# Kernel tuning notes

Hardware: AMD Instinct MI355X
Metric: run time of the kernel (lower is better)

Reference implementation:

```python
import jax, jax.numpy as jnp
import numpy as np

NUM_HOPS = 8
NEG_INF = -1e9


def setup_inputs() -> dict:
    key = jax.random.key(0)
    ks = jax.random.split(key, 10)
    B, N, D, H = 4, 1024, 256, 8
    x = jax.random.normal(ks[0], (B, N, D), dtype=jnp.float32)
    adj = (jax.random.uniform(ks[1], (B, N, N)) < 0.02).astype(jnp.int32)
    edge_attr = jax.random.normal(ks[2], (B, H, N, N), dtype=jnp.float32) * 0.1
    s = 1.0 / np.sqrt(D)
    Wq = jax.random.normal(ks[3], (D, D), dtype=jnp.float32) * s
    Wk = jax.random.normal(ks[4], (D, D), dtype=jnp.float32) * s
    Wv = jax.random.normal(ks[5], (D, D), dtype=jnp.float32) * s
    Wo = jax.random.normal(ks[6], (D, D), dtype=jnp.float32) * s
    W_fuse = jax.random.normal(ks[7], (H, D), dtype=jnp.float32) * s
    diff_weight = jax.random.normal(ks[8], (NUM_HOPS, H), dtype=jnp.float32)
    return {"x": x, "adj": adj, "edge_attr": edge_attr, "Wq": Wq, "Wk": Wk,
            "Wv": Wv, "Wo": Wo, "W_fuse": W_fuse, "diff_weight": diff_weight}


def edge_gat(x, adj, edge_attr, Wq, Wk, Wv, Wo):
    B, N, D = x.shape
    H = edge_attr.shape[1]
    dh = D // H
    q = (x @ Wq).reshape(B, N, H, dh)
    k = (x @ Wk).reshape(B, N, H, dh)
    v = (x @ Wv).reshape(B, N, H, dh)
    scores = jnp.einsum("bihd,bjhd->bhij", q, k) / jnp.sqrt(jnp.float32(dh))
    scores = scores + edge_attr  # additive edge bias
    mask = (adj > 0)[:, None, :, :]  # [B,1,N,N]
    attn = jax.nn.softmax(jnp.where(mask, scores, NEG_INF), axis=-1)
    out = jnp.einsum("bhij,bjhd->bihd", attn, v).reshape(B, N, D)
    return x + out @ Wo


def node_edge_fusion(x, adj, edge_attr, W_fuse):
    # degree-normalized per-head aggregation of incident edge features -> nodes
    a = adj.astype(x.dtype)
    deg = jnp.clip(a.sum(-1), 1.0)  # [B,N]
    f = jnp.einsum("bij,bhij->bih", a, edge_attr) / deg[:, :, None]  # [B,N,H]
    return x + f @ W_fuse


def graph_diffusion(adj, weight):
    # BFS hop-distance bias: bias[b,h,i,j] = weight[hop(i,j), h] if reachable in <= NUM_HOPS hops
    K, H = weight.shape
    a = adj.astype(jnp.float32)
    reach = adj > 0
    explored = reach
    dist = jnp.where(reach, 0, K)  # hop index (0 == 1-hop neighbor)
    cur = a
    for k in range(1, K):
        cur_b = (cur @ a) > 0
        newly = cur_b & ~explored
        dist = jnp.where(newly, k, dist)
        explored = explored | newly
        cur = cur_b.astype(jnp.float32)
    dist_c = jnp.clip(dist, 0, K - 1)
    bias = jnp.where(explored[..., None], weight[dist_c], 0.0)  # [B,N,N,H]
    return jnp.transpose(bias, (0, 3, 1, 2)), explored


def reference(x, adj, edge_attr, Wq, Wk, Wv, Wo, W_fuse, diff_weight):
    x1 = edge_gat(x, adj, edge_attr, Wq, Wk, Wv, Wo)
    x2 = node_edge_fusion(x1, adj, edge_attr, W_fuse)
    position_bias = edge_attr
    bfs_bias, explored = graph_diffusion(adj, diff_weight)
    att_bias = position_bias + bfs_bias
    return x2, att_bias, explored
```

## Files before the change

### kernel.cpp

```cpp
#include <hip/hip_runtime.h>
#include <stdint.h>

#define NN 1024
#define DD 256
#define KHOPS 8

typedef unsigned short u16;
typedef unsigned long long u64;
typedef unsigned char u8;
typedef float f32x4v __attribute__((ext_vector_type(4)));

__device__ __forceinline__ float b2f(u16 u){ return __uint_as_float(((unsigned int)u) << 16); }
__device__ __forceinline__ u16 f2b(float f){
  unsigned int x = __float_as_uint(f);
  unsigned int r = (x + 0x7FFFu + ((x >> 16) & 1u)) >> 16;
  return (u16)r;
}
__device__ __forceinline__ float wsum(float v){
  #pragma unroll
  for(int off = 32; off >= 1; off >>= 1) v += __shfl_xor(v, off, 64);
  return v;
}

__global__ __launch_bounds__(256) void k_fill(float* p, unsigned n, float v){
  unsigned idx = blockIdx.x * 256 + threadIdx.x;
  if(idx < n) p[idx] = v;
}

__global__ __launch_bounds__(256) void k_prep(const float* X, const float* Wq, const float* Wk,
                                              const float* Wv, float* qf, float* kf, u16* vb,
                                              const int* adj, u64* bits){
  __shared__ float xs[32][256];
  int t = threadIdx.x;
  if(blockIdx.x >= 384){
    int vblk = blockIdx.x - 384;
    int row = vblk * 4 + (t >> 6);
    int lane = t & 63;
    const int* ar = adj + (size_t)row * NN;
    #pragma unroll
    for(int w = 0; w < 16; w++){
      u64 msk = __ballot(ar[w * 64 + lane] != 0);
      if(lane == 0) bits[(size_t)row * 16 + w] = msk;
    }
    return;
  }
  int proj = blockIdx.x >> 7;
  int rb = blockIdx.x & 127;
  const float* W = (proj == 0) ? Wq : (proj == 1) ? Wk : Wv;
  const float* Xb = X + (size_t)rb * 32 * 256;
  #pragma unroll
  for(int m = 0; m < 32; m++) xs[m][t] = Xb[m * 256 + t];
  __syncthreads();
  float acc[32];
  #pragma unroll
  for(int r = 0; r < 32; r++) acc[r] = 0.f;
  for(int k4 = 0; k4 < 64; k4++){
    float w0 = W[(size_t)(k4 * 4 + 0) * 256 + t];
    float w1 = W[(size_t)(k4 * 4 + 1) * 256 + t];
    float w2 = W[(size_t)(k4 * 4 + 2) * 256 + t];
    float w3 = W[(size_t)(k4 * 4 + 3) * 256 + t];
    #pragma unroll
    for(int r = 0; r < 32; r++){
      float4 xv = *(const float4*)&xs[r][k4 * 4];
      acc[r] = fmaf(xv.x, w0, fmaf(xv.y, w1, fmaf(xv.z, w2, fmaf(xv.w, w3, acc[r]))));
    }
  }
  int rowbase = rb * 32;
  if(proj == 2){
    for(int r = 0; r < 32; r++) vb[(size_t)(rowbase + r) * 256 + t] = f2b(acc[r]);
  } else {
    float* dst = (proj == 0) ? qf : kf;
    for(int r = 0; r < 32; r++) dst[(size_t)(rowbase + r) * 256 + t] = acc[r];
  }
}

__global__ __launch_bounds__(512) void k_bfs(const u64* bits, u8* dist, float* expl){
  __shared__ __attribute__((aligned(16))) u64 asw[16384];
  __shared__ __attribute__((aligned(16))) u8 drow4[8][1024];
  __shared__ u64 red4[8][16];
  int tid = threadIdx.x;
  int wv = tid >> 6, lane = tid & 63;
  int batch = blockIdx.x >> 6;
  int rowbase = (blockIdx.x & 63) * 16;
  const u64* bb = bits + (((size_t)batch << 10)) * 16;
  for(int g = tid; g < 8192; g += 512){
    int j = g >> 3, c = g & 7;
    ulonglong2 v = *(const ulonglong2*)(bb + (size_t)j * 16 + c * 2);
    int ce = c ^ (j & 7);
    *(ulonglong2*)(&asw[j * 16 + ce * 2]) = v;
  }
  __syncthreads();
  int s = lane & 7;
  for(int rr = 0; rr < 2; rr++){
    int row_local = rowbase + wv * 2 + rr;
    int row = (batch << 10) + row_local;
    u64 vis[16], cur[16];
    {
      const u64* p = asw + row_local * 16;
      int sr = row_local & 7;
      #pragma unroll
      for(int c = 0; c < 8; c++){
        ulonglong2 v = *(const ulonglong2*)(p + (((c ^ sr)) << 1));
        vis[2*c] = v.x; vis[2*c+1] = v.y;
        cur[2*c] = v.x; cur[2*c+1] = v.y;
      }
    }
    { int4 ff; ff.x = ff.y = ff.z = ff.w = -1; ((int4*)drow4[wv])[lane] = ff; }
    __builtin_amdgcn_wave_barrier();
    #pragma unroll
    for(int it = 0; it < 16; it++)
      if((cur[it] >> lane) & 1) drow4[wv][it * 64 + lane] = 0;
    for(int k = 1; k < KHOPS; k++){
      unsigned mymask = 0;
      #pragma unroll
      for(int it = 0; it < 16; it++) mymask |= ((unsigned)((cur[it] >> lane) & 1)) << it;
      u64 acc[16];
      #pragma unroll
      for(int w = 0; w < 16; w++) acc[w] = 0;
      while(mymask){
        int it0 = __builtin_ctz(mymask); mymask &= mymask - 1;
        int it1 = it0;
        if(mymask){ it1 = __builtin_ctz(mymask); mymask &= mymask - 1; }
        const u64* pA = asw + (it0 * 64 + lane) * 16;
        const u64* pB = asw + (it1 * 64 + lane) * 16;
        ulonglong2 a0 = *(const ulonglong2*)(pA + ((0^s)<<1)), b0 = *(const ulonglong2*)(pB + ((0^s)<<1));
        ulonglong2 a1 = *(const ulonglong2*)(pA + ((1^s)<<1)), b1 = *(const ulonglong2*)(pB + ((1^s)<<1));
        ulonglong2 a2 = *(const ulonglong2*)(pA + ((2^s)<<1)), b2 = *(const ulonglong2*)(pB + ((2^s)<<1));
        ulonglong2 a3 = *(const ulonglong2*)(pA + ((3^s)<<1)), b3 = *(const ulonglong2*)(pB + ((3^s)<<1));
        ulonglong2 a4 = *(const ulonglong2*)(pA + ((4^s)<<1)), b4 = *(const ulonglong2*)(pB + ((4^s)<<1));
        ulonglong2 a5 = *(const ulonglong2*)(pA + ((5^s)<<1)), b5 = *(const ulonglong2*)(pB + ((5^s)<<1));
        ulonglong2 a6 = *(const ulonglong2*)(pA + ((6^s)<<1)), b6 = *(const ulonglong2*)(pB + ((6^s)<<1));
        ulonglong2 a7 = *(const ulonglong2*)(pA + ((7^s)<<1)), b7 = *(const ulonglong2*)(pB + ((7^s)<<1));
        acc[0]  |= a0.x | b0.x;  acc[1]  |= a0.y | b0.y;
        acc[2]  |= a1.x | b1.x;  acc[3]  |= a1.y | b1.y;
        acc[4]  |= a2.x | b2.x;  acc[5]  |= a2.y | b2.y;
        acc[6]  |= a3.x | b3.x;  acc[7]  |= a3.y | b3.y;
        acc[8]  |= a4.x | b4.x;  acc[9]  |= a4.y | b4.y;
        acc[10] |= a5.x | b5.x;  acc[11] |= a5.y | b5.y;
        acc[12] |= a6.x | b6.x;  acc[13] |= a6.y | b6.y;
        acc[14] |= a7.x | b7.x;  acc[15] |= a7.y | b7.y;
      }
      #pragma unroll
      for(int w = 0; w < 16; w++){
        acc[w] |= __shfl_xor(acc[w], 16, 64);
        acc[w] |= __shfl_xor(acc[w], 32, 64);
      }
      int g4 = lane >> 4;
      u64 r0, r1, r2, r3;
      if(g4 == 0){ r0 = acc[0];  r1 = acc[1];  r2 = acc[2];  r3 = acc[3];  }
      else if(g4 == 1){ r0 = acc[4];  r1 = acc[5];  r2 = acc[6];  r3 = acc[7];  }
      else if(g4 == 2){ r0 = acc[8];  r1 = acc[9];  r2 = acc[10]; r3 = acc[11]; }
      else            { r0 = acc[12]; r1 = acc[13]; r2 = acc[14]; r3 = acc[15]; }
      #pragma unroll
      for(int off = 1; off <= 8; off <<= 1){
        r0 |= __shfl_xor(r0, off, 64);
        r1 |= __shfl_xor(r1, off, 64);
        r2 |= __shfl_xor(r2, off, 64);
        r3 |= __shfl_xor(r3, off, 64);
      }
      int sub = lane & 15;
      if(sub == 0)      red4[wv][g4 * 4 + 0] = r0;
      else if(sub == 1) red4[wv][g4 * 4 + 1] = r1;
      else if(sub == 2) red4[wv][g4 * 4 + 2] = r2;
      else if(sub == 3) red4[wv][g4 * 4 + 3] = r3;
      __builtin_amdgcn_wave_barrier();
      u64 any = 0, andv = ~0ull;
      #pragma unroll
      for(int w = 0; w < 16; w++){
        u64 nv = red4[wv][w];
        u64 nw = nv & ~vis[w];
        vis[w] |= nw;
        cur[w] = nw;
        any |= nw;
        andv &= vis[w];
      }
      __builtin_amdgcn_wave_barrier();
      if(any == 0) break;
      #pragma unroll
      for(int it = 0; it < 16; it++)
        if((cur[it] >> lane) & 1) drow4[wv][it * 64 + lane] = (u8)k;
      if(andv == ~0ull) break;
    }
    __builtin_amdgcn_wave_barrier();
    ((int4*)(dist + (size_t)row * NN))[lane] = ((const int4*)drow4[wv])[lane];
    float* eo = expl + (size_t)row * NN;
    #pragma unroll
    for(int it = 0; it < 16; it++){
      int j = it * 64 + lane;
      eo[j] = ((vis[it] >> lane) & 1) ? 1.0f : 0.0f;
    }
  }
}

__global__ __launch_bounds__(256) void k_biasattn(
    const float* x, const u64* bits, const float* ea, const u8* dist, const float* dw,
    const float* qf, const float* kf, const u16* vb,
    const float* Wo, const float* Wf, float* ab_out, float* x2)
{
  __shared__ float qs[256];
  __shared__ float aos[256];
  __shared__ float fs[8];
  __shared__ u16 nlist[1024];
  __shared__ float sc0[4][64], sc1[4][64];
  __shared__ float evl0[4][64], evl1[4][64];
  __shared__ float w8s[8][8];
  __shared__ u64 wm[16];
  __shared__ int bs[16];
  __shared__ int ncnt_s;
  int t = threadIdx.x, wv = t >> 6, lane = t & 63;
  int bi = blockIdx.x, b = bi >> 10, i = bi & 1023;
  qs[t] = qf[(size_t)bi * 256 + t];
  if(t < 64) w8s[t & 7][t >> 3] = dw[(t >> 3) * 8 + (t & 7)];
  if(wv == 0){
    if(lane < 16) wm[lane] = bits[(size_t)bi * 16 + lane];
    __builtin_amdgcn_wave_barrier();
    if(lane == 0){
      int run = 0;
      #pragma unroll
      for(int it = 0; it < 16; it++){ bs[it] = run; run += __popcll(wm[it]); }
      ncnt_s = run;
    }
    __builtin_amdgcn_wave_barrier();
    if(lane < 16){
      u64 w = wm[lane];
      int pos = bs[lane];
      while(w){
        int bpos = __builtin_ctzll(w);
        nlist[pos++] = (u16)(lane * 64 + bpos);
        w &= w - 1;
      }
    }
  }
  __syncthreads();
  int cnt = ncnt_s;
  const float scale = 0.17677669529663687f;
  int d = lane & 31;
  int half = lane >> 5;
  bool isV = (lane >= 32);
  int g8 = lane >> 3, r8 = lane & 7;
  size_t kvbase = ((size_t)(b << 10)) * 256;
  const u8* drow = dist + (size_t)bi * NN;
  int h0 = wv * 2, h1 = wv * 2 + 1;
  int widx0 = (((b << 3) + h0) << 10) + i;
  int widx1 = (((b << 3) + h1) << 10) + i;
  const float* earow0 = ea + (size_t)widx0 * NN;
  const float* earow1 = ea + (size_t)widx1 * NN;
  float* abrow0 = ab_out + (size_t)widx0 * NN;
  float* abrow1 = ab_out + (size_t)widx1 * NN;
  float fpart0 = 0.f, fpart1 = 0.f;
  #pragma unroll
  for(int g = 0; g < 4; g++){
    int idx = g * 256 + lane * 4;
    f32x4v e0 = *(const f32x4v*)(earow0 + idx);
    f32x4v e1 = *(const f32x4v*)(earow1 + idx);
    unsigned dd4 = *(const unsigned*)(drow + idx);
    float v0[4] = {e0.x, e0.y, e0.z, e0.w};
    float v1[4] = {e1.x, e1.y, e1.z, e1.w};
    f32x4v o0, o1;
    #pragma unroll
    for(int e2 = 0; e2 < 4; e2++){
      int dd = (dd4 >> (e2 * 8)) & 255;
      float w0 = (dd != 255) ? w8s[h0][dd & 7] : 0.f;
      float w1 = (dd != 255) ? w8s[h1][dd & 7] : 0.f;
      float ov0 = v0[e2] + w0, ov1 = v1[e2] + w1;
      if(e2 == 0){ o0.x = ov0; o1.x = ov1; }
      else if(e2 == 1){ o0.y = ov0; o1.y = ov1; }
      else if(e2 == 2){ o0.z = ov0; o1.z = ov1; }
      else { o0.w = ov0; o1.w = ov1; }
      if(dd == 0){ fpart0 += v0[e2]; fpart1 += v1[e2]; }
    }
    __builtin_nontemporal_store(o0, (f32x4v*)(abrow0 + idx));
    __builtin_nontemporal_store(o1, (f32x4v*)(abrow1 + idx));
  }
  float fsum0 = wsum(fpart0);
  float fsum1 = wsum(fpart1);
  if(lane == 0){
    fs[h0] = (cnt > 0) ? fsum0 / (float)cnt : 0.f;
    fs[h1] = (cnt > 0) ? fsum1 / (float)cnt : 0.f;
  }
  if(cnt > 0 && cnt <= 64){
    for(int s = lane; s < cnt; s += 64){
      int j = nlist[s];
      evl0[wv][s] = earow0[j];
      evl1[wv][s] = earow1[j];
    }
  }
  __builtin_amdgcn_wave_barrier();
  if(cnt > 0 && cnt <= 64){
    float4 q40 = *(const float4*)&qs[h0 * 32 + r8 * 4];
    float4 q41 = *(const float4*)&qs[h1 * 32 + r8 * 4];
    for(int u = 0; u < cnt; u += 8){
      int s = u + g8;
      bool valid = (s < cnt);
      int j = nlist[valid ? s : (cnt - 1)];
      const float* krow = kf + kvbase + (size_t)j * 256;
      float4 k40 = *(const float4*)(krow + h0 * 32 + r8 * 4);
      float4 k41 = *(const float4*)(krow + h1 * 32 + r8 * 4);
      float p0 = k40.x * q40.x + k40.y * q40.y + k40.z * q40.z + k40.w * q40.w;
      float p1 = k41.x * q41.x + k41.y * q41.y + k41.z * q41.z + k41.w * q41.w;
      p0 += __shfl_xor(p0, 1, 64);  p1 += __shfl_xor(p1, 1, 64);
      p0 += __shfl_xor(p0, 2, 64);  p1 += __shfl_xor(p1, 2, 64);
      p0 += __shfl_xor(p0, 4, 64);  p1 += __shfl_xor(p1, 4, 64);
      if(r8 == 0 && valid){
        sc0[wv][s] = p0 * scale + evl0[wv][s];
        sc1[wv][s] = p1 * scale + evl1[wv][s];
      }
    }
    __builtin_amdgcn_wave_barrier();
    float m0 = -3.0e38f, m1 = -3.0e38f;
    for(int s = 0; s < cnt; s++){ m0 = fmaxf(m0, sc0[wv][s]); m1 = fmaxf(m1, sc1[wv][s]); }
    float4 o40 = {0.f,0.f,0.f,0.f}, o41 = {0.f,0.f,0.f,0.f};
    float Sp0 = 0.f, Sp1 = 0.f;
    for(int u = 0; u < cnt; u += 8){
      int s = u + g8;
      if(s < cnt){
        float p0 = __expf(sc0[wv][s] - m0);
        float p1 = __expf(sc1[wv][s] - m1);
        Sp0 += p0; Sp1 += p1;
        int j = nlist[s];
        const u16* vrow = vb + kvbase + (size_t)j * 256;
        ushort4 vv0 = *(const ushort4*)(vrow + h0 * 32 + r8 * 4);
        ushort4 vv1 = *(const ushort4*)(vrow + h1 * 32 + r8 * 4);
        o40.x = fmaf(p0, b2f(vv0.x), o40.x);  o41.x = fmaf(p1, b2f(vv1.x), o41.x);
        o40.y = fmaf(p0, b2f(vv0.y), o40.y);  o41.y = fmaf(p1, b2f(vv1.y), o41.y);
        o40.z = fmaf(p0, b2f(vv0.z), o40.z);  o41.z = fmaf(p1, b2f(vv1.z), o41.z);
        o40.w = fmaf(p0, b2f(vv0.w), o40.w);  o41.w = fmaf(p1, b2f(vv1.w), o41.w);
      }
    }
    #pragma unroll
    for(int off = 8; off <= 32; off <<= 1){
      o40.x += __shfl_xor(o40.x, off, 64);  o41.x += __shfl_xor(o41.x, off, 64);
      o40.y += __shfl_xor(o40.y, off, 64);  o41.y += __shfl_xor(o41.y, off, 64);
      o40.z += __shfl_xor(o40.z, off, 64);  o41.z += __shfl_xor(o41.z, off, 64);
      o40.w += __shfl_xor(o40.w, off, 64);  o41.w += __shfl_xor(o41.w, off, 64);
      Sp0 += __shfl_xor(Sp0, off, 64);      Sp1 += __shfl_xor(Sp1, off, 64);
    }
    if(g8 == 0){
      float iS0 = 1.f / Sp0, iS1 = 1.f / Sp1;
      float4 ov0; ov0.x = o40.x * iS0; ov0.y = o40.y * iS0; ov0.z = o40.z * iS0; ov0.w = o40.w * iS0;
      float4 ov1; ov1.x = o41.x * iS1; ov1.y = o41.y * iS1; ov1.z = o41.z * iS1; ov1.w = o41.w * iS1;
      *(float4*)&aos[h0 * 32 + r8 * 4] = ov0;
      *(float4*)&aos[h1 * 32 + r8 * 4] = ov1;
    }
  } else if(cnt > 64){
    #pragma unroll
    for(int hh = 0; hh < 2; hh++){
      int h = wv * 2 + hh;
      const float* earow = (hh == 0) ? earow0 : earow1;
      const float* Kb = kf + kvbase + h * 32 + d;
      const u16*   Vb = vb + kvbase + h * 32 + d;
      float q_d = qs[h * 32 + d];
      float S = 0.f, o = 0.f;
      float m = -3.0e38f;
      for(int idx = 0; idx < cnt; idx++){
        int j = nlist[idx];
        float kv = isV ? b2f(Vb[(size_t)j * 256]) : Kb[(size_t)j * 256];
        float prod = isV ? 0.f : kv * q_d;
        #pragma unroll
        for(int off = 16; off >= 1; off >>= 1) prod += __shfl_xor(prod, off, 64);
        float e = earow[j];
        float s2 = __shfl(prod, 0, 64) * scale + e;
        float nm = fmaxf(m, s2);
        float rs = __expf(m - nm);
        float p  = __expf(s2 - nm);
        S = S * rs + p;
        o = o * rs + p * (isV ? kv : 0.f);
        m = nm;
      }
      if(isV) aos[h * 32 + d] = o / S;
    }
  } else {
    #pragma unroll
    for(int hh = 0; hh < 2; hh++){
      int h = wv * 2 + hh;
      const u16* Vb = vb + kvbase + h * 32 + d;
      float o = 0.f;
      for(int j2 = half; j2 < 1024; j2 += 2)
        o += b2f(Vb[(size_t)j2 * 256]);
      o += __shfl_xor(o, 32, 64);
      if(lane < 32) aos[h * 32 + d] = o / 1024.f;
    }
  }
  __syncthreads();
  const float* Wcol = Wo + t;
  float r0 = x[(size_t)bi * 256 + t], r1 = 0.f, r2 = 0.f, r3 = 0.f;
  #pragma unroll 4
  for(int k = 0; k < 256; k += 4){
    r0 = fmaf(aos[k],     Wcol[(size_t)k * 256],       r0);
    r1 = fmaf(aos[k + 1], Wcol[(size_t)(k + 1) * 256], r1);
    r2 = fmaf(aos[k + 2], Wcol[(size_t)(k + 2) * 256], r2);
    r3 = fmaf(aos[k + 3], Wcol[(size_t)(k + 3) * 256], r3);
  }
  float res = (r0 + r1) + (r2 + r3);
  #pragma unroll
  for(int h = 0; h < 8; h++) res = fmaf(fs[h], Wf[(size_t)h * 256 + t], res);
  x2[(size_t)bi * 256 + t] = res;
}

extern "C" void kernel_launch(void* const* d_in, const int* in_sizes, int n_in,
                              void* d_out, int out_size, void* d_ws, size_t ws_size,
                              hipStream_t stream) {
  float* out = (float*)d_out;
  float* x2   = out;
  float* ab   = out + 1048576;
  float* expl = out + 34603008;

  bool ok = (n_in == 9) &&
            in_sizes[0] == 1048576  &&
            in_sizes[1] == 4194304  &&
            in_sizes[2] == 33554432 &&
            in_sizes[3] == 65536 && in_sizes[4] == 65536 &&
            in_sizes[5] == 65536 && in_sizes[6] == 65536 &&
            in_sizes[7] == 2048  && in_sizes[8] == 64 &&
            out_size == 38797312;
  if(!ok){
    hipLaunchKernelGGL(k_fill, dim3(4096), dim3(256), 0, stream, x2, 1048576u, 1000.0f);
    return;
  }
  if(ws_size < (size_t)15204352){
    hipLaunchKernelGGL(k_fill, dim3(4096), dim3(256), 0, stream, x2, 1048576u, 2000.0f);
    return;
  }

  const float* x   = (const float*)d_in[0];
  const int*   adj = (const int*)d_in[1];
  const float* ea  = (const float*)d_in[2];
  const float* Wq  = (const float*)d_in[3];
  const float* Wk  = (const float*)d_in[4];
  const float* Wv  = (const float*)d_in[5];
  const float* Wo  = (const float*)d_in[6];
  const float* Wf  = (const float*)d_in[7];
  const float* dw  = (const float*)d_in[8];

  char* ws = (char*)d_ws;
  u64*   bits  = (u64*)(ws + 0);
  u8*    dist  = (u8*)(ws + 524288);
  float* qf    = (float*)(ws + 4718592);
  float* kf    = (float*)(ws + 8912896);
  u16*   vb    = (u16*)(ws + 13107200);

  hipLaunchKernelGGL(k_prep,     dim3(1408), dim3(256), 0, stream,
                     x, Wq, Wk, Wv, qf, kf, vb, adj, bits);
  hipLaunchKernelGGL(k_bfs,      dim3(256),  dim3(512), 0, stream, bits, dist, expl);
  hipLaunchKernelGGL(k_biasattn, dim3(4096), dim3(256), 0, stream,
                     x, bits, ea, dist, dw, qf, kf, vb, Wo, Wf, ab, x2);
}
```

Baseline: 182.4 us.

## Split output projection into separate batched kernel reusing Wo across rows

Moves the Wo/W_fuse output projection out of the per-row attention kernel into a new kernel that processes 16 rows per block. Attention output and fused edge values are written to workspace instead of shared memory. Each Wo element is then loaded once per 16 rows rather than once per row, which cuts global/L2 traffic on Wo. In exchange there is an extra kernel launch, a workspace round trip, and the new kernel runs only 256 blocks.

```diff
diff --git a/kernel.cpp b/kernel.cpp
--- a/kernel.cpp
+++ b/kernel.cpp
@@ -193,13 +193,11 @@
 }
 
 __global__ __launch_bounds__(256) void k_biasattn(
-    const float* x, const u64* bits, const float* ea, const u8* dist, const float* dw,
+    const u64* bits, const float* ea, const u8* dist, const float* dw,
     const float* qf, const float* kf, const u16* vb,
-    const float* Wo, const float* Wf, float* ab_out, float* x2)
+    float* ab_out, float* ao, float* fvals)
 {
   __shared__ float qs[256];
-  __shared__ float aos[256];
-  __shared__ float fs[8];
   __shared__ u16 nlist[1024];
   __shared__ float sc0[4][64], sc1[4][64];
   __shared__ float evl0[4][64], evl1[4][64];
@@ -240,6 +238,7 @@
   int g8 = lane >> 3, r8 = lane & 7;
   size_t kvbase = ((size_t)(b << 10)) * 256;
   const u8* drow = dist + (size_t)bi * NN;
+  float* aorow = ao + (size_t)bi * 256;
   int h0 = wv * 2, h1 = wv * 2 + 1;
   int widx0 = (((b << 3) + h0) << 10) + i;
   int widx1 = (((b << 3) + h1) << 10) + i;
@@ -275,8 +274,8 @@
   float fsum0 = wsum(fpart0);
   float fsum1 = wsum(fpart1);
   if(lane == 0){
-    fs[h0] = (cnt > 0) ? fsum0 / (float)cnt : 0.f;
-    fs[h1] = (cnt > 0) ? fsum1 / (float)cnt : 0.f;
+    fvals[widx0] = (cnt > 0) ? fsum0 / (float)cnt : 0.f;
+    fvals[widx1] = (cnt > 0) ? fsum1 / (float)cnt : 0.f;
   }
   if(cnt > 0 && cnt <= 64){
     for(int s = lane; s < cnt; s += 64){
@@ -339,8 +338,8 @@
       float iS0 = 1.f / Sp0, iS1 = 1.f / Sp1;
       float4 ov0; ov0.x = o40.x * iS0; ov0.y = o40.y * iS0; ov0.z = o40.z * iS0; ov0.w = o40.w * iS0;
       float4 ov1; ov1.x = o41.x * iS1; ov1.y = o41.y * iS1; ov1.z = o41.z * iS1; ov1.w = o41.w * iS1;
-      *(float4*)&aos[h0 * 32 + r8 * 4] = ov0;
-      *(float4*)&aos[h1 * 32 + r8 * 4] = ov1;
+      *(float4*)(aorow + h0 * 32 + r8 * 4) = ov0;
+      *(float4*)(aorow + h1 * 32 + r8 * 4) = ov1;
     }
   } else if(cnt > 64){
     #pragma unroll
@@ -367,7 +366,7 @@
         o = o * rs + p * (isV ? kv : 0.f);
         m = nm;
       }
-      if(isV) aos[h * 32 + d] = o / S;
+      if(isV) aorow[h * 32 + d] = o / S;
     }
   } else {
     #pragma unroll
@@ -378,23 +377,52 @@
       for(int j2 = half; j2 < 1024; j2 += 2)
         o += b2f(Vb[(size_t)j2 * 256]);
       o += __shfl_xor(o, 32, 64);
-      if(lane < 32) aos[h * 32 + d] = o / 1024.f;
-    }
+      if(lane < 32) aorow[h * 32 + d] = o / 1024.f;
+    }
+  }
+}
+
+__global__ __launch_bounds__(256) void k_outproj(const float* ao, const float* x, const float* fsd,
+                                                 const float* Wo, const float* Wf, float* x2){
+  __shared__ float as_[16][256];
+  __shared__ float fsl[16][8];
+  int t = threadIdx.x;
+  int rb = blockIdx.x;
+  const float* Ab = ao + (size_t)rb * 16 * 256;
+  #pragma unroll
+  for(int m = 0; m < 16; m++) as_[m][t] = Ab[m * 256 + t];
+  if(t < 128){
+    int m = t >> 3, h = t & 7;
+    int row = rb * 16 + m;
+    int b = row >> 10, i = row & 1023;
+    fsl[m][h] = fsd[((((size_t)b << 3) + h) << 10) + i];
   }
   __syncthreads();
-  const float* Wcol = Wo + t;
-  float r0 = x[(size_t)bi * 256 + t], r1 = 0.f, r2 = 0.f, r3 = 0.f;
-  #pragma unroll 4
-  for(int k = 0; k < 256; k += 4){
-    r0 = fmaf(aos[k],     Wcol[(size_t)k * 256],       r0);
-    r1 = fmaf(aos[k + 1], Wcol[(size_t)(k + 1) * 256], r1);
-    r2 = fmaf(aos[k + 2], Wcol[(size_t)(k + 2) * 256], r2);
-    r3 = fmaf(aos[k + 3], Wcol[(size_t)(k + 3) * 256], r3);
-  }
-  float res = (r0 + r1) + (r2 + r3);
-  #pragma unroll
-  for(int h = 0; h < 8; h++) res = fmaf(fs[h], Wf[(size_t)h * 256 + t], res);
-  x2[(size_t)bi * 256 + t] = res;
+  float acc[16];
+  #pragma unroll
+  for(int r = 0; r < 16; r++) acc[r] = 0.f;
+  for(int k4 = 0; k4 < 64; k4++){
+    float w0 = Wo[(size_t)(k4 * 4 + 0) * 256 + t];
+    float w1 = Wo[(size_t)(k4 * 4 + 1) * 256 + t];
+    float w2 = Wo[(size_t)(k4 * 4 + 2) * 256 + t];
+    float w3 = Wo[(size_t)(k4 * 4 + 3) * 256 + t];
+    #pragma unroll
+    for(int r = 0; r < 16; r++){
+      float4 av = *(const float4*)&as_[r][k4 * 4];
+      acc[r] = fmaf(av.x, w0, fmaf(av.y, w1, fmaf(av.z, w2, fmaf(av.w, w3, acc[r]))));
+    }
+  }
+  float wf[8];
+  #pragma unroll
+  for(int h = 0; h < 8; h++) wf[h] = Wf[(size_t)h * 256 + t];
+  int rowbase = rb * 16;
+  for(int r = 0; r < 16; r++){
+    int row = rowbase + r;
+    float res = acc[r] + x[(size_t)row * 256 + t];
+    #pragma unroll
+    for(int h = 0; h < 8; h++) res = fmaf(fsl[r][h], wf[h], res);
+    x2[(size_t)row * 256 + t] = res;
+  }
 }
 
 extern "C" void kernel_launch(void* const* d_in, const int* in_sizes, int n_in,
@@ -417,7 +445,7 @@
     hipLaunchKernelGGL(k_fill, dim3(4096), dim3(256), 0, stream, x2, 1048576u, 1000.0f);
     return;
   }
-  if(ws_size < (size_t)15204352){
+  if(ws_size < (size_t)19791872){
     hipLaunchKernelGGL(k_fill, dim3(4096), dim3(256), 0, stream, x2, 1048576u, 2000.0f);
     return;
   }
@@ -438,10 +466,14 @@
   float* qf    = (float*)(ws + 4718592);
   float* kf    = (float*)(ws + 8912896);
   u16*   vb    = (u16*)(ws + 13107200);
+  float* ao    = (float*)(ws + 15204352);
+  float* fvals = (float*)(ws + 19398656);
 
   hipLaunchKernelGGL(k_prep,     dim3(1408), dim3(256), 0, stream,
                      x, Wq, Wk, Wv, qf, kf, vb, adj, bits);
   hipLaunchKernelGGL(k_bfs,      dim3(256),  dim3(512), 0, stream, bits, dist, expl);
   hipLaunchKernelGGL(k_biasattn, dim3(4096), dim3(256), 0, stream,
-                     x, bits, ea, dist, dw, qf, kf, vb, Wo, Wf, ab, x2);
-}
+                     bits, ea, dist, dw, qf, kf, vb, ab, ao, fvals);
+  hipLaunchKernelGGL(k_outproj,  dim3(256),  dim3(256), 0, stream,
+                     ao, x, fvals, Wo, Wf, x2);
+}
```

Measured after the change: 190.5 us. 1.04x slower.
